# Performance work log

Hardware: AMD Instinct MI355X
Metric: run time of the kernel (lower is better)

The kernel has to match this reference:

```python
import jax, jax.numpy as jnp
import numpy as np

B, T, L = 256, 1024, 64
INIT = 0.1


def setup_inputs() -> dict:
    key = jax.random.key(0)
    k1, k2, k3, k4, k5 = jax.random.split(key, 5)
    scores = jax.random.normal(k1, (B, T, L), dtype=jnp.float32)
    targets = jax.random.randint(k2, (B, T), 0, L)
    start = jax.random.uniform(k3, (L,), dtype=jnp.float32, minval=-INIT, maxval=INIT)
    T_mat = jax.random.uniform(k4, (L, L), dtype=jnp.float32, minval=-INIT, maxval=INIT)
    end = jax.random.uniform(k5, (L,), dtype=jnp.float32, minval=-INIT, maxval=INIT)
    return {"scores": scores, "targets": targets, "start": start, "T_mat": T_mat, "end": end}


def reference(scores, targets, start, T_mat, end):
    # scores: [B,T,L], targets: [B,T] int, start/end: [L], T_mat: [L,L] with T_mat[cur, prev]
    Ttr = T_mat.T  # [prev, cur]

    # --- normalizers via forward algorithm (scan over time) ---
    prev0 = start[None, :] + scores[:, 0]  # [B,L]

    def step(prev, emit):  # prev [B,L], emit [B,L]
        cur = prev[:, :, None] + emit[:, None, :] + Ttr[None, :, :]  # [B,prev,cur]
        return jax.scipy.special.logsumexp(cur, axis=1), None

    emits_t = jnp.swapaxes(scores, 0, 1)[1:]  # [T-1,B,L]
    prev, _ = jax.lax.scan(step, prev0, emits_t)
    normalizers = jax.scipy.special.logsumexp(prev + end[None, :], axis=1)  # [B]

    # --- gold path score ---
    emits = jnp.take_along_axis(scores, targets[:, :, None], axis=2).squeeze(2).sum(axis=1)  # [B]
    trans = (start[targets[:, 0]]
             + T_mat[targets[:, 1:], targets[:, :-1]].sum(axis=1)
             + end[targets[:, -1]])  # [B]
    target_scores = emits + trans

    return (normalizers - target_scores).mean()
```

## Files before the change

### kernel.cpp

```cpp
#include <hip/hip_runtime.h>

#define NB 256
#define NT 1024
#define NL 64

typedef __fp16 h2v __attribute__((ext_vector_type(2)));

__device__ __forceinline__ float rfl_f(float v) {
  return __builtin_bit_cast(float, __builtin_amdgcn_readfirstlane(__builtin_bit_cast(int, v)));
}

__device__ __forceinline__ float dpp_xor1(float v) {
  int i = __builtin_bit_cast(int, v);
  int r = __builtin_amdgcn_update_dpp(i, i, 0xB1, 0xF, 0xF, false);
  return __builtin_bit_cast(float, r);
}

#define DOT4(P, B)                                                            \
  s0 = __builtin_amdgcn_fdot2(__builtin_bit_cast(h2v, (P).x), Rh[(B) + 0], s0, false); \
  s1 = __builtin_amdgcn_fdot2(__builtin_bit_cast(h2v, (P).y), Rh[(B) + 1], s1, false); \
  s2 = __builtin_amdgcn_fdot2(__builtin_bit_cast(h2v, (P).z), Rh[(B) + 2], s2, false); \
  s3 = __builtin_amdgcn_fdot2(__builtin_bit_cast(h2v, (P).w), Rh[(B) + 3], s3, false);

#define CRF_STEP(EF)                                                          \
  do {                                                                        \
    float wn = dpp_xor1(w);                                                   \
    h2v pk = __builtin_amdgcn_cvt_pkrtz(w, wn);                               \
    lb[wslot] = __builtin_bit_cast(int, pk);                                  \
    int4 P0 = lbv[0], P1 = lbv[1], P2 = lbv[2], P3 = lbv[3];                  \
    int4 P4 = lbv[4], P5 = lbv[5], P6 = lbv[6], P7 = lbv[7];                  \
    int e5 = (P0.x >> 10) & 0x1f;                                             \
    float K = __builtin_bit_cast(float, (130 - e5) << 23);                    \
    float KE = K * (EF);                                                      \
    e2 += e5 - 3;                                                             \
    float s0 = 0.f, s1 = 0.f, s2 = 0.f, s3 = 0.f;                             \
    DOT4(P0, 0); DOT4(P1, 4); DOT4(P2, 8); DOT4(P3, 12);                      \
    DOT4(P4, 16); DOT4(P5, 20); DOT4(P6, 24); DOT4(P7, 28);                   \
    w = ((s0 + s1) + (s2 + s3)) * KE;                                         \
  } while (0)

__global__ __launch_bounds__(64) void fb_kernel(const float* __restrict__ scores,
                                                const int* __restrict__ targets,
                                                const float* __restrict__ start,
                                                const float* __restrict__ Tm,
                                                const float* __restrict__ endv,
                                                float* __restrict__ wsA,
                                                float* __restrict__ wsB,
                                                float* __restrict__ wsG) {
  const int lane = threadIdx.x;
  const int bb = blockIdx.x;

  if (bb >= 2 * NB) {
    const int b = bb - 2 * NB;
    const int* tg = targets + b * NT;
    const float* sc = scores + (size_t)b * NT * NL;
    float acc = 0.f;
    for (int t = lane; t < NT; t += 64) {
      int c = tg[t];
      acc += sc[t * NL + c];
      if (t > 0) acc += Tm[c * NL + tg[t - 1]];
    }
#pragma unroll
    for (int off = 32; off > 0; off >>= 1) acc += __shfl_xor(acc, off, 64);
    if (lane == 0) wsG[b] = acc + start[tg[0]] + endv[tg[NT - 1]];
    return;
  }

  __shared__ int4 lbv_s[16];
  int* lb = (int*)lbv_s;
  const int4* lbv = lbv_s;
  const int wslot = (lane & 1) * 32 + (lane >> 1);

  const bool bwd = bb >= NB;
  const int b = bwd ? bb - NB : bb;
  const float* sc = scores + (size_t)b * NT * NL;
  const float LN2 = 0.69314718055994530942f;

  const float* Tb = bwd ? (Tm + lane) : (Tm + lane * NL);
  const int str = bwd ? NL : 1;
  h2v Rh[32];
#pragma unroll
  for (int k = 0; k < 32; k++)
    Rh[k] = __builtin_amdgcn_cvt_pkrtz(__expf(Tb[(2 * k) * str]),
                                       __expf(Tb[(2 * k + 1) * str]));

  if (!bwd) {
    float a0 = start[lane] + sc[lane];
    float m0 = rfl_f(a0);
    float w = __expf(a0 - m0) * 16.f;
    int e2 = -4;

    float buf[4];
#pragma unroll
    for (int k = 0; k < 4; k++) buf[k] = sc[(1 + k) * NL + lane];

    for (int i = 0; i < 128; i++) {
      float nb4[4];
      int tb = 5 + 4 * i;
#pragma unroll
      for (int k = 0; k < 4; k++) nb4[k] = sc[(tb + k) * NL + lane];
      float Ev[4];
#pragma unroll
      for (int k = 0; k < 4; k++) Ev[k] = __expf(buf[k]);
      CRF_STEP(Ev[0]);
      CRF_STEP(Ev[1]);
      CRF_STEP(Ev[2]);
      CRF_STEP(Ev[3]);
#pragma unroll
      for (int k = 0; k < 4; k++) buf[k] = nb4[k];
    }
    wsA[lane * NB + b] = m0 + (float)e2 * LN2 + __logf(w);
  } else {
    float a0 = endv[lane] + sc[(NT - 1) * NL + lane];
    float m0 = rfl_f(a0);
    float w = __expf(a0 - m0) * 16.f;
    int e2 = -4;

    float buf[4];
#pragma unroll
    for (int k = 0; k < 4; k++) buf[k] = sc[(1022 - k) * NL + lane];

    for (int i = 0; i < 127; i++) {
      float nb4[4];
      int tb = 1018 - 4 * i;
#pragma unroll
      for (int k = 0; k < 4; k++) nb4[k] = sc[(tb - k) * NL + lane];
      float Ev[4];
#pragma unroll
      for (int k = 0; k < 4; k++) Ev[k] = __expf(buf[k]);
      CRF_STEP(Ev[0]);
      CRF_STEP(Ev[1]);
      CRF_STEP(Ev[2]);
      CRF_STEP(Ev[3]);
#pragma unroll
      for (int k = 0; k < 4; k++) buf[k] = nb4[k];
    }
    CRF_STEP(__expf(sc[514 * NL + lane]));
    CRF_STEP(__expf(sc[513 * NL + lane]));
    CRF_STEP(1.0f);
    wsB[lane * NB + b] = m0 + (float)e2 * LN2 + __logf(w);
  }
}

__global__ __launch_bounds__(256) void combine_kernel(const float* __restrict__ wsA,
                                                      const float* __restrict__ wsB,
                                                      const float* __restrict__ wsG,
                                                      float* __restrict__ out) {
  const int b = threadIdx.x;
  float m = -INFINITY;
#pragma unroll
  for (int j = 0; j < NL; j++) m = fmaxf(m, wsA[j * NB + b] + wsB[j * NB + b]);
  float s = 0.f;
#pragma unroll
  for (int j = 0; j < NL; j++) s += __expf(wsA[j * NB + b] + wsB[j * NB + b] - m);
  float loss = (m + __logf(s)) - wsG[b];
#pragma unroll
  for (int off = 32; off > 0; off >>= 1) loss += __shfl_xor(loss, off, 64);
  __shared__ float red[4];
  if ((b & 63) == 0) red[b >> 6] = loss;
  __syncthreads();
  if (b == 0) out[0] = (red[0] + red[1] + red[2] + red[3]) * (1.0f / NB);
}

extern "C" void kernel_launch(void* const* d_in, const int* in_sizes, int n_in,
                              void* d_out, int out_size, void* d_ws, size_t ws_size,
                              hipStream_t stream) {
  const float* scores = (const float*)d_in[0];
  const int* targets = (const int*)d_in[1];
  const float* start = (const float*)d_in[2];
  const float* Tm = (const float*)d_in[3];
  const float* endv = (const float*)d_in[4];
  float* out = (float*)d_out;

  float* wsA = (float*)d_ws;
  float* wsB = wsA + NB * NL;
  float* wsG = wsB + NB * NL;

  fb_kernel<<<3 * NB, 64, 0, stream>>>(scores, targets, start, Tm, endv, wsA, wsB, wsG);
  combine_kernel<<<1, 256, 0, stream>>>(wsA, wsB, wsG, out);
}
```

Measured before the change: 178.3 us.

## Interleave forward and backward recursions in one wave per batch

Each wavefront now runs both the forward and backward scaled recursions for one sequence, interleaving their LDS broadcast and fdot2 matvec steps so that one chain's latency hides the other's. This halves the number of recursion workgroups and holds both transition tables in registers, with launch_bounds(64,1). The per-step exponent correction is folded into a single constant at the end. The cost is higher register pressure and fewer waves available to hide latency across the GPU.

```diff
diff --git a/kernel.cpp b/kernel.cpp
--- a/kernel.cpp
+++ b/kernel.cpp
@@ -16,42 +16,51 @@
   return __builtin_bit_cast(float, r);
 }
 
-#define DOT4(P, B)                                                            \
-  s0 = __builtin_amdgcn_fdot2(__builtin_bit_cast(h2v, (P).x), Rh[(B) + 0], s0, false); \
-  s1 = __builtin_amdgcn_fdot2(__builtin_bit_cast(h2v, (P).y), Rh[(B) + 1], s1, false); \
-  s2 = __builtin_amdgcn_fdot2(__builtin_bit_cast(h2v, (P).z), Rh[(B) + 2], s2, false); \
-  s3 = __builtin_amdgcn_fdot2(__builtin_bit_cast(h2v, (P).w), Rh[(B) + 3], s3, false);
+#define CRF_BCAST(PFX, W, LB, LBV)                                            \
+  float PFX##wn = dpp_xor1(W);                                                \
+  h2v PFX##pk = __builtin_amdgcn_cvt_pkrtz(W, PFX##wn);                       \
+  LB[slot] = __builtin_bit_cast(int, PFX##pk);                                \
+  int4 PFX##P0 = LBV[0], PFX##P1 = LBV[1], PFX##P2 = LBV[2], PFX##P3 = LBV[3];\
+  int4 PFX##P4 = LBV[4], PFX##P5 = LBV[5], PFX##P6 = LBV[6], PFX##P7 = LBV[7];
 
-#define CRF_STEP(EF)                                                          \
-  do {                                                                        \
-    float wn = dpp_xor1(w);                                                   \
-    h2v pk = __builtin_amdgcn_cvt_pkrtz(w, wn);                               \
-    lb[wslot] = __builtin_bit_cast(int, pk);                                  \
-    int4 P0 = lbv[0], P1 = lbv[1], P2 = lbv[2], P3 = lbv[3];                  \
-    int4 P4 = lbv[4], P5 = lbv[5], P6 = lbv[6], P7 = lbv[7];                  \
-    int e5 = (P0.x >> 10) & 0x1f;                                             \
-    float K = __builtin_bit_cast(float, (130 - e5) << 23);                    \
-    float KE = K * (EF);                                                      \
-    e2 += e5 - 3;                                                             \
-    float s0 = 0.f, s1 = 0.f, s2 = 0.f, s3 = 0.f;                             \
-    DOT4(P0, 0); DOT4(P1, 4); DOT4(P2, 8); DOT4(P3, 12);                      \
-    DOT4(P4, 16); DOT4(P5, 20); DOT4(P6, 24); DOT4(P7, 28);                   \
-    w = ((s0 + s1) + (s2 + s3)) * KE;                                         \
-  } while (0)
+#define DOT4P(PFX, P, B, RT)                                                  \
+  PFX##s0 = __builtin_amdgcn_fdot2(__builtin_bit_cast(h2v, (P).x), RT[(B) + 0], PFX##s0, false); \
+  PFX##s1 = __builtin_amdgcn_fdot2(__builtin_bit_cast(h2v, (P).y), RT[(B) + 1], PFX##s1, false); \
+  PFX##s2 = __builtin_amdgcn_fdot2(__builtin_bit_cast(h2v, (P).z), RT[(B) + 2], PFX##s2, false); \
+  PFX##s3 = __builtin_amdgcn_fdot2(__builtin_bit_cast(h2v, (P).w), RT[(B) + 3], PFX##s3, false);
 
-__global__ __launch_bounds__(64) void fb_kernel(const float* __restrict__ scores,
-                                                const int* __restrict__ targets,
-                                                const float* __restrict__ start,
-                                                const float* __restrict__ Tm,
-                                                const float* __restrict__ endv,
-                                                float* __restrict__ wsA,
-                                                float* __restrict__ wsB,
-                                                float* __restrict__ wsG) {
+#define CRF_MATVEC(PFX, W, E2, RT, EF)                                        \
+  int PFX##e5 = (PFX##P0.x >> 10) & 0x1f;                                     \
+  float PFX##K = __builtin_bit_cast(float, (130 - PFX##e5) << 23);            \
+  E2 += PFX##e5;                                                              \
+  float PFX##s0 = 0.f, PFX##s1 = 0.f, PFX##s2 = 0.f, PFX##s3 = 0.f;           \
+  DOT4P(PFX, PFX##P0, 0, RT) DOT4P(PFX, PFX##P1, 4, RT)                       \
+  DOT4P(PFX, PFX##P2, 8, RT) DOT4P(PFX, PFX##P3, 12, RT)                      \
+  DOT4P(PFX, PFX##P4, 16, RT) DOT4P(PFX, PFX##P5, 20, RT)                     \
+  DOT4P(PFX, PFX##P6, 24, RT) DOT4P(PFX, PFX##P7, 28, RT)                     \
+  W = ((PFX##s0 + PFX##s1) + (PFX##s2 + PFX##s3)) * (PFX##K * (EF));
+
+#define STEP_PAIR(EFF, EFB)                                                   \
+  {                                                                           \
+    CRF_BCAST(F_, wF, lbF, lbvF)                                              \
+    CRF_BCAST(B_, wB, lbB, lbvB)                                              \
+    CRF_MATVEC(F_, wF, e2F, Rf, EFF)                                          \
+    CRF_MATVEC(B_, wB, e2B, Rb, EFB)                                          \
+  }
+
+__global__ __launch_bounds__(64, 1) void fb_kernel(const float* __restrict__ scores,
+                                                   const int* __restrict__ targets,
+                                                   const float* __restrict__ start,
+                                                   const float* __restrict__ Tm,
+                                                   const float* __restrict__ endv,
+                                                   float* __restrict__ wsA,
+                                                   float* __restrict__ wsB,
+                                                   float* __restrict__ wsG) {
   const int lane = threadIdx.x;
   const int bb = blockIdx.x;
 
-  if (bb >= 2 * NB) {
-    const int b = bb - 2 * NB;
+  if (bb >= NB) {
+    const int b = bb - NB;
     const int* tg = targets + b * NT;
     const float* sc = scores + (size_t)b * NT * NL;
     float acc = 0.f;
@@ -66,80 +75,83 @@
     return;
   }
 
-  __shared__ int4 lbv_s[16];
-  int* lb = (int*)lbv_s;
-  const int4* lbv = lbv_s;
-  const int wslot = (lane & 1) * 32 + (lane >> 1);
+  __shared__ int4 lds_s[32];
+  int* lbF = (int*)lds_s;
+  int* lbB = (int*)(lds_s + 16);
+  const int4* lbvF = lds_s;
+  const int4* lbvB = lds_s + 16;
+  const int slot = (lane & 1) * 32 + (lane >> 1);
 
-  const bool bwd = bb >= NB;
-  const int b = bwd ? bb - NB : bb;
+  const int b = bb;
   const float* sc = scores + (size_t)b * NT * NL;
   const float LN2 = 0.69314718055994530942f;
 
-  const float* Tb = bwd ? (Tm + lane) : (Tm + lane * NL);
-  const int str = bwd ? NL : 1;
-  h2v Rh[32];
+  h2v Rf[32], Rb[32];
 #pragma unroll
-  for (int k = 0; k < 32; k++)
-    Rh[k] = __builtin_amdgcn_cvt_pkrtz(__expf(Tb[(2 * k) * str]),
-                                       __expf(Tb[(2 * k + 1) * str]));
+  for (int k = 0; k < 32; k++) {
+    Rf[k] = __builtin_amdgcn_cvt_pkrtz(__expf(Tm[lane * NL + 2 * k]),
+                                       __expf(Tm[lane * NL + 2 * k + 1]));
+    Rb[k] = __builtin_amdgcn_cvt_pkrtz(__expf(Tm[(2 * k) * NL + lane]),
+                                       __expf(Tm[(2 * k + 1) * NL + lane]));
+  }
 
-  if (!bwd) {
-    float a0 = start[lane] + sc[lane];
-    float m0 = rfl_f(a0);
-    float w = __expf(a0 - m0) * 16.f;
-    int e2 = -4;
+  float aF = start[lane] + sc[lane];
+  float mF = rfl_f(aF);
+  float wF = __expf(aF - mF) * 16.f;
+  int e2F = -4;
 
-    float buf[4];
+  float aB = endv[lane] + sc[(NT - 1) * NL + lane];
+  float mB = rfl_f(aB);
+  float wB = __expf(aB - mB) * 16.f;
+  int e2B = -4;
+
+  float bufF[4], bufB[4];
 #pragma unroll
-    for (int k = 0; k < 4; k++) buf[k] = sc[(1 + k) * NL + lane];
+  for (int k = 0; k < 4; k++) {
+    bufF[k] = sc[(1 + k) * NL + lane];
+    bufB[k] = sc[(1022 - k) * NL + lane];
+  }
 
-    for (int i = 0; i < 128; i++) {
-      float nb4[4];
-      int tb = 5 + 4 * i;
+  for (int i = 0; i < 127; i++) {
+    float nbF[4], nbB[4];
+    int tf = 5 + 4 * i, tb = 1018 - 4 * i;
 #pragma unroll
-      for (int k = 0; k < 4; k++) nb4[k] = sc[(tb + k) * NL + lane];
-      float Ev[4];
+    for (int k = 0; k < 4; k++) {
+      nbF[k] = sc[(tf + k) * NL + lane];
+      nbB[k] = sc[(tb - k) * NL + lane];
+    }
+    float EvF[4], EvB[4];
 #pragma unroll
-      for (int k = 0; k < 4; k++) Ev[k] = __expf(buf[k]);
-      CRF_STEP(Ev[0]);
-      CRF_STEP(Ev[1]);
-      CRF_STEP(Ev[2]);
-      CRF_STEP(Ev[3]);
+    for (int k = 0; k < 4; k++) {
+      EvF[k] = __expf(bufF[k]);
+      EvB[k] = __expf(bufB[k]);
+    }
+    STEP_PAIR(EvF[0], EvB[0])
+    STEP_PAIR(EvF[1], EvB[1])
+    STEP_PAIR(EvF[2], EvB[2])
+    STEP_PAIR(EvF[3], EvB[3])
 #pragma unroll
-      for (int k = 0; k < 4; k++) buf[k] = nb4[k];
+    for (int k = 0; k < 4; k++) {
+      bufF[k] = nbF[k];
+      bufB[k] = nbB[k];
     }
-    wsA[lane * NB + b] = m0 + (float)e2 * LN2 + __logf(w);
-  } else {
-    float a0 = endv[lane] + sc[(NT - 1) * NL + lane];
-    float m0 = rfl_f(a0);
-    float w = __expf(a0 - m0) * 16.f;
-    int e2 = -4;
+  }
 
-    float buf[4];
-#pragma unroll
-    for (int k = 0; k < 4; k++) buf[k] = sc[(1022 - k) * NL + lane];
+  {
+    float EvF0 = __expf(bufF[0]), EvF1 = __expf(bufF[1]);
+    float EvF2 = __expf(bufF[2]), EvF3 = __expf(bufF[3]);
+    float EvB0 = __expf(bufB[0]), EvB1 = __expf(bufB[1]);
+    STEP_PAIR(EvF0, EvB0)
+    STEP_PAIR(EvF1, EvB1)
+    STEP_PAIR(EvF2, 1.0f)
+    {
+      CRF_BCAST(F_, wF, lbF, lbvF)
+      CRF_MATVEC(F_, wF, e2F, Rf, EvF3)
+    }
+  }
 
-    for (int i = 0; i < 127; i++) {
-      float nb4[4];
-      int tb = 1018 - 4 * i;
-#pragma unroll
-      for (int k = 0; k < 4; k++) nb4[k] = sc[(tb - k) * NL + lane];
-      float Ev[4];
-#pragma unroll
-      for (int k = 0; k < 4; k++) Ev[k] = __expf(buf[k]);
-      CRF_STEP(Ev[0]);
-      CRF_STEP(Ev[1]);
-      CRF_STEP(Ev[2]);
-      CRF_STEP(Ev[3]);
-#pragma unroll
-      for (int k = 0; k < 4; k++) buf[k] = nb4[k];
-    }
-    CRF_STEP(__expf(sc[514 * NL + lane]));
-    CRF_STEP(__expf(sc[513 * NL + lane]));
-    CRF_STEP(1.0f);
-    wsB[lane * NB + b] = m0 + (float)e2 * LN2 + __logf(w);
-  }
+  wsA[lane * NB + b] = mF + (float)(e2F - 3 * 512) * LN2 + __logf(wF);
+  wsB[lane * NB + b] = mB + (float)(e2B - 3 * 511) * LN2 + __logf(wB);
 }
 
 __global__ __launch_bounds__(256) void combine_kernel(const float* __restrict__ wsA,
@@ -176,6 +188,6 @@
   float* wsB = wsA + NB * NL;
   float* wsG = wsB + NB * NL;
 
-  fb_kernel<<<3 * NB, 64, 0, stream>>>(scores, targets, start, Tm, endv, wsA, wsB, wsG);
+  fb_kernel<<<2 * NB, 64, 0, stream>>>(scores, targets, start, Tm, endv, wsA, wsB, wsG);
   combine_kernel<<<1, 256, 0, stream>>>(wsA, wsB, wsG, out);
 }
```

Result: slower. 246.1 us (+38.0%).
